# Performance work log

Measured on AMD Instinct MI355X. Metric: run time of the kernel, lower is better.

## Reference

```python
import jax, jax.numpy as jnp
import numpy as np

N_A, N_B = 50000, 10000
E = 300000
IN_F, HID, BEL_OUT, INC_OUT = 256, 256, 128, 128


def _gconv(x_src, W, b, src, dst, n_src, n_dst):
    """DGL GraphConv with norm='both': D_in^{-1/2} A D_out^{-1/2} X W + b, degs clamped to >=1."""
    ones = jnp.ones(src.shape[0], x_src.dtype)
    deg_out = jnp.maximum(jax.ops.segment_sum(ones, src, num_segments=n_src), 1.0)
    deg_in = jnp.maximum(jax.ops.segment_sum(ones, dst, num_segments=n_dst), 1.0)
    h = (x_src * jax.lax.rsqrt(deg_out)[:, None]) @ W        # [n_src, out]
    agg = jax.ops.segment_sum(h[src], dst, num_segments=n_dst)  # scatter-add messages
    return agg * jax.lax.rsqrt(deg_in)[:, None] + b


def setup_inputs() -> dict:
    key = jax.random.key(0)
    ks = jax.random.split(key, 12)
    s = 1.0 / np.sqrt(IN_F)
    sh = 1.0 / np.sqrt(HID)
    return {
        "x_a": jax.random.normal(ks[0], (N_A, IN_F), jnp.float32),
        "x_b": jax.random.normal(ks[1], (N_B, IN_F), jnp.float32),
        "W1_bel": jax.random.normal(ks[2], (IN_F, HID), jnp.float32) * s,
        "b1_bel": jnp.zeros((HID,), jnp.float32),
        "W1_inc": jax.random.normal(ks[3], (IN_F, HID), jnp.float32) * s,
        "b1_inc": jnp.zeros((HID,), jnp.float32),
        "W2_bel": jax.random.normal(ks[4], (HID, BEL_OUT), jnp.float32) * sh,
        "b2_bel": jnp.zeros((BEL_OUT,), jnp.float32),
        "W2_inc": jax.random.normal(ks[5], (HID, INC_OUT), jnp.float32) * sh,
        "b2_inc": jnp.zeros((INC_OUT,), jnp.float32),
        "bel_src": jax.random.randint(ks[6], (E,), 0, N_A, jnp.int32),
        "bel_dst": jax.random.randint(ks[7], (E,), 0, N_B, jnp.int32),
        "inc_src": jax.random.randint(ks[8], (E,), 0, N_B, jnp.int32),
        "inc_dst": jax.random.randint(ks[9], (E,), 0, N_A, jnp.int32),
    }


def reference(x_a, x_b, W1_bel, b1_bel, W1_inc, b1_inc, W2_bel, b2_bel,
              W2_inc, b2_inc, bel_src, bel_dst, inc_src, inc_dst):
    n_a, n_b = x_a.shape[0], x_b.shape[0]
    # layer 1 (HeteroGraphConv, mean over a single relation per dst type = identity)
    h_b = _gconv(x_a, W1_bel, b1_bel, bel_src, bel_dst, n_a, n_b)  # 'belongs_to': A->B
    h_a = _gconv(x_b, W1_inc, b1_inc, inc_src, inc_dst, n_b, n_a)  # 'including' : B->A
    h_a = jax.nn.relu(h_a)
    h_b = jax.nn.relu(h_b)
    # layer 2
    out_b = _gconv(h_a, W2_bel, b2_bel, bel_src, bel_dst, n_a, n_b)  # [N_B, bel_out]
    out_a = _gconv(h_b, W2_inc, b2_inc, inc_src, inc_dst, n_b, n_a)  # [N_A, inc_out]
    return out_a, out_b
```

## Files before the change

kernel.cpp:

```cpp
#include <hip/hip_runtime.h>


#define NA 50000
#define NB 10000
#define NE 300000
#define HB 1172
#define CVTB 400

typedef unsigned short u16;
typedef unsigned int u32;
typedef __attribute__((ext_vector_type(8))) short short8;
typedef __attribute__((ext_vector_type(4))) float f32x4;
typedef __attribute__((ext_vector_type(2))) float f32x2;
typedef __attribute__((ext_vector_type(4))) unsigned short u16x4;

__device__ __forceinline__ float bf2f(u16 h){
  union { u32 u; float f; } x; x.u = ((u32)h) << 16; return x.f;
}
__device__ __forceinline__ u16 f2bf(float f){
  union { float f; u32 u; } x; x.f = f;
  u32 r = (x.u + 0x7FFFu + ((x.u >> 16) & 1u)) >> 16;
  return (u16)r;
}

__global__ __launch_bounds__(256) void setup0_kernel(
    int* __restrict__ z, int nz,
    const float* __restrict__ W1b, const float* __restrict__ W1i,
    const float* __restrict__ W2b, const float* __restrict__ W2i,
    u16* __restrict__ pwh, u16* __restrict__ pwl){
  int g = blockIdx.x * blockDim.x + threadIdx.x;
  int s = gridDim.x * blockDim.x;
  for (int i = g; i < nz; i += s) z[i] = 0;
  const int total = 65536 + 65536 + 32768 + 32768;
  for (int t = g; t < total; t += s){
    const float* W; int N; int tt;
    if (t < 65536)       { W = W1b; N = 256; tt = t; }
    else if (t < 131072) { W = W1i; N = 256; tt = t - 65536; }
    else if (t < 163840) { W = W2b; N = 128; tt = t - 131072; }
    else                 { W = W2i; N = 128; tt = t - 163840; }
    int j = tt & 7, lane = (tt >> 3) & 63, tile = tt >> 9;
    int nT = N >> 4;
    int nt = tile % nT, kt = tile / nT;
    int k = kt * 32 + ((lane >> 4) << 3) + j;
    int n = nt * 16 + (lane & 15);
    float v = W[k * N + n];
    u16 hi = f2bf(v);
    pwh[t] = hi;
    pwl[t] = f2bf(v - bf2f(hi));
  }
}

__global__ __launch_bounds__(256) void histcvt_kernel(
    const int* __restrict__ bs, const int* __restrict__ bd,
    const int* __restrict__ isc, const int* __restrict__ idt,
    int* __restrict__ c_bs, int* __restrict__ c_bd,
    int* __restrict__ c_is, int* __restrict__ c_id,
    int* __restrict__ rank_bel, int* __restrict__ rank_inc,
    const float* __restrict__ xa, u16* __restrict__ xa16){
  if (blockIdx.x < HB){
    int g = blockIdx.x * blockDim.x + threadIdx.x;
    int s = HB * blockDim.x;
    for (int e = g; e < NE; e += s){
      atomicAdd(&c_bs[bs[e]], 1);
      rank_bel[e] = atomicAdd(&c_bd[bd[e]], 1);
      atomicAdd(&c_is[isc[e]], 1);
      rank_inc[e] = atomicAdd(&c_id[idt[e]], 1);
    }
  } else {
    int g = ((blockIdx.x - HB) * blockDim.x + threadIdx.x) * 4;
    int s = CVTB * blockDim.x * 4;
    for (int i = g; i < NA * 256; i += s){
      float4 v = *(const float4*)(xa + i);
      u16x4 o;
      o.x = f2bf(v.x); o.y = f2bf(v.y); o.z = f2bf(v.z); o.w = f2bf(v.w);
      __builtin_nontemporal_store(o, (u16x4*)(xa16 + i));
    }
  }
}

__global__ __launch_bounds__(1024) void scan_scales_kernel(
    const int* __restrict__ c_bs, const int* __restrict__ c_bd,
    const int* __restrict__ c_is, const int* __restrict__ c_id,
    int* __restrict__ off_bel, int* __restrict__ off_inc,
    float* __restrict__ s_ob, float* __restrict__ s_ib,
    float* __restrict__ s_oi, float* __restrict__ s_ii){
  if (blockIdx.x >= 2){
    int g = (blockIdx.x - 2) * blockDim.x + threadIdx.x;
    int s = (gridDim.x - 2) * blockDim.x;
    for (int i = g; i < NA; i += s){
      int a = c_bs[i]; s_ob[i] = rsqrtf((float)(a > 1 ? a : 1));
      int b = c_id[i]; s_ii[i] = rsqrtf((float)(b > 1 ? b : 1));
      if (i < NB){
        int c = c_bd[i]; s_ib[i] = rsqrtf((float)(c > 1 ? c : 1));
        int d = c_is[i]; s_oi[i] = rsqrtf((float)(d > 1 ? d : 1));
      }
    }
    return;
  }
  const int* cnt; int* off; int n;
  if (blockIdx.x == 0){ cnt = c_bd; off = off_bel; n = NB; }
  else                { cnt = c_id; off = off_inc; n = NA; }
  __shared__ int wsum[16];
  __shared__ int carry, chunkTot;
  int tid = threadIdx.x, lane = tid & 63, wid = tid >> 6;
  if (tid == 0) carry = 0;
  __syncthreads();
  for (int base = 0; base < n; base += 4096){
    int i0 = base + tid * 4;
    int v[4];
#pragma unroll
    for (int r = 0; r < 4; ++r){ int idx = i0 + r; v[r] = (idx < n) ? cnt[idx] : 0; }
    int s = v[0] + v[1] + v[2] + v[3];
    int x = s;
#pragma unroll
    for (int d = 1; d < 64; d <<= 1){ int t = __shfl_up(x, d, 64); if (lane >= d) x += t; }
    if (lane == 63) wsum[wid] = x;
    __syncthreads();
    if (wid == 0){
      int ws = (lane < 16) ? wsum[lane] : 0;
#pragma unroll
      for (int d = 1; d < 16; d <<= 1){ int t = __shfl_up(ws, d, 64); if (lane >= d) ws += t; }
      if (lane < 16) wsum[lane] = ws;
      if (lane == 15) chunkTot = ws;
    }
    __syncthreads();
    int waveBase = (wid == 0) ? 0 : wsum[wid - 1];
    int run = carry + waveBase + (x - s);
#pragma unroll
    for (int r = 0; r < 4; ++r){ int idx = i0 + r; if (idx < n) off[idx] = run; run += v[r]; }
    __syncthreads();
    if (tid == 0) carry += chunkTot;
    __syncthreads();
  }
  if (tid == 0) off[n] = carry;
}

__global__ __launch_bounds__(256) void fill_kernel(
    const int* __restrict__ bs, const int* __restrict__ bd,
    const int* __restrict__ isc, const int* __restrict__ idt,
    const int* __restrict__ rank_bel, const int* __restrict__ rank_inc,
    const int* __restrict__ off_bel, const int* __restrict__ off_inc,
    int* __restrict__ csr_bel, int* __restrict__ csr_inc){
  int g = blockIdx.x * blockDim.x + threadIdx.x;
  int s = gridDim.x * blockDim.x;
  for (int e = g; e < NE; e += s){
    csr_bel[off_bel[bd[e]] + rank_bel[e]] = bs[e];
    csr_inc[off_inc[idt[e]] + rank_inc[e]] = isc[e];
  }
}

__global__ __launch_bounds__(256) void agg_bel_kernel(
    const u16* __restrict__ X, const float* __restrict__ ss,
    const int* __restrict__ off, const int* __restrict__ csr,
    float* __restrict__ Pf, int nDst){
  int wave = blockIdx.x * 4 + (threadIdx.x >> 6);
  int lane = threadIdx.x & 63;
  if (wave >= nDst) return;
  int b0 = off[wave], b1 = off[wave + 1];
  int deg = b1 - b0;
  int part = lane >> 5;
  int cl = lane & 31;
  int c = cl * 8;
  float acc[8];
#pragma unroll
  for (int q = 0; q < 8; ++q) acc[q] = 0.f;
  int idx = 0; float sc = 0.f;
  if (lane < deg){
    idx = csr[b0 + lane];
    sc = ss ? ss[idx] : 1.f;
  }
  int lim = deg < 64 ? deg : 64;
  for (int u = 0; u < lim; u += 8){
    const u16* addr[4]; float w[4];
#pragma unroll
    for (int k = 0; k < 4; ++k){
      int e = u + k * 2 + part;
      int t = e < lim ? e : 0;
      int s0 = __shfl(idx, t, 64);
      float c0 = __shfl(sc, t, 64);
      w[k] = e < lim ? c0 : 0.f;
      addr[k] = X + (size_t)s0 * 256 + c;
    }
    short8 v[4];
#pragma unroll
    for (int k = 0; k < 4; ++k) v[k] = *(const short8*)addr[k];
#pragma unroll
    for (int k = 0; k < 4; ++k)
#pragma unroll
      for (int q = 0; q < 8; ++q) acc[q] += bf2f((u16)v[k][q]) * w[k];
  }
  for (int j = b0 + 64 + part; j < b1; j += 2){
    int s0 = csr[j];
    float c0 = ss ? ss[s0] : 1.f;
    short8 v0 = *(const short8*)(X + (size_t)s0 * 256 + c);
#pragma unroll
    for (int q = 0; q < 8; ++q) acc[q] += bf2f((u16)v0[q]) * c0;
  }
#pragma unroll
  for (int q = 0; q < 8; ++q) acc[q] += __shfl_xor(acc[q], 32, 64);
  if (part == 0){
    f32x4 f0 = {acc[0], acc[1], acc[2], acc[3]};
    f32x4 f1 = {acc[4], acc[5], acc[6], acc[7]};
    __builtin_nontemporal_store(f0, (f32x4*)(Pf + (size_t)wave * 256 + c));
    __builtin_nontemporal_store(f1, (f32x4*)(Pf + (size_t)wave * 256 + c + 4));
  }
}

__global__ __launch_bounds__(256) void agg_inc2_kernel(
    const u16* __restrict__ G12, const int* __restrict__ off,
    const int* __restrict__ csr,
    const float* __restrict__ s_ii, const float* __restrict__ s_ob,
    const float* __restrict__ b1i, const float* __restrict__ b2i,
    u16* __restrict__ Ha, float* __restrict__ outa){
  int wave = blockIdx.x * 4 + (threadIdx.x >> 6);
  int lane = threadIdx.x & 63;
  if (wave >= NA) return;
  int b0 = off[wave], b1 = off[wave + 1];
  int deg = b1 - b0;
  int c1 = lane * 4;
  int c2 = lane * 2;
  float acc[6];
#pragma unroll
  for (int q = 0; q < 6; ++q) acc[q] = 0.f;
  int idx = 0;
  if (lane < deg) idx = csr[b0 + lane];
  int lim = deg < 64 ? deg : 64;
  for (int u = 0; u < lim; u += 4){
    ushort4 va[4]; ushort2 vb[4]; float w[4];
#pragma unroll
    for (int k = 0; k < 4; ++k){
      int e = u + k;
      int t = e < lim ? e : 0;
      int se = __shfl(idx, t, 64);
      w[k] = e < lim ? 1.f : 0.f;
      const u16* r = G12 + (size_t)se * 384;
      va[k] = *(const ushort4*)(r + c1);
      vb[k] = *(const ushort2*)(r + 256 + c2);
    }
#pragma unroll
    for (int k = 0; k < 4; ++k){
      acc[0] += bf2f(va[k].x) * w[k];
      acc[1] += bf2f(va[k].y) * w[k];
      acc[2] += bf2f(va[k].z) * w[k];
      acc[3] += bf2f(va[k].w) * w[k];
      acc[4] += bf2f(vb[k].x) * w[k];
      acc[5] += bf2f(vb[k].y) * w[k];
    }
  }
  for (int j = b0 + 64; j < b1; ++j){
    int se = csr[j];
    const u16* r = G12 + (size_t)se * 384;
    ushort4 va = *(const ushort4*)(r + c1);
    ushort2 vb = *(const ushort2*)(r + 256 + c2);
    acc[0] += bf2f(va.x); acc[1] += bf2f(va.y);
    acc[2] += bf2f(va.z); acc[3] += bf2f(va.w);
    acc[4] += bf2f(vb.x); acc[5] += bf2f(vb.y);
  }
  float sii = s_ii[wave], sob = s_ob[wave];
  float4 bb1 = *(const float4*)(b1i + c1);
  f32x2 bb2 = *(const f32x2*)(b2i + c2);
  u16x4 o1;
  o1.x = f2bf(fmaxf(acc[0] * sii + bb1.x, 0.f) * sob);
  o1.y = f2bf(fmaxf(acc[1] * sii + bb1.y, 0.f) * sob);
  o1.z = f2bf(fmaxf(acc[2] * sii + bb1.z, 0.f) * sob);
  o1.w = f2bf(fmaxf(acc[3] * sii + bb1.w, 0.f) * sob);
  __builtin_nontemporal_store(o1, (u16x4*)(Ha + (size_t)wave * 256 + c1));
  f32x2 o2 = {acc[4] * sii + bb2.x, acc[5] * sii + bb2.y};
  __builtin_nontemporal_store(o2, (f32x2*)(outa + (size_t)wave * 128 + c2));
}

__global__ __launch_bounds__(256) void gemm_kernel(
    const float* __restrict__ A,
    const u16* __restrict__ PWH, const u16* __restrict__ PWL,
    const float* __restrict__ bias, const float* __restrict__ rs,
    float* __restrict__ Cf, u16* __restrict__ C16,
    int M, int nT, int wpsShift, int doRelu, int ldC, int colOff){
  int wave = blockIdx.x * 4 + (threadIdx.x >> 6);
  int lane = threadIdx.x & 63;
  int strips = M >> 4;
  int strip = wave >> wpsShift;
  if (strip >= strips) return;
  int slice = wave & ((1 << wpsShift) - 1);
  int ntPer = nT >> wpsShift;
  int ntStart = slice * ntPer;
  int r16 = lane & 15, quad = lane >> 4;
  int m0 = strip << 4;
  const float* aBase = A + (size_t)(m0 + r16) * 256 + quad * 8;
  short8 ah[8], al[8];
#pragma unroll
  for (int kt = 0; kt < 8; ++kt){
    float4 p0 = *(const float4*)(aBase + kt * 32);
    float4 p1 = *(const float4*)(aBase + kt * 32 + 4);
    float v[8] = {p0.x, p0.y, p0.z, p0.w, p1.x, p1.y, p1.z, p1.w};
    short8 h, l;
#pragma unroll
    for (int j = 0; j < 8; ++j){
      u16 hb = f2bf(v[j]);
      h[j] = (short)hb;
      l[j] = (short)f2bf(v[j] - bf2f(hb));
    }
    ah[kt] = h; al[kt] = l;
  }
  float rscale[4];
#pragma unroll
  for (int r = 0; r < 4; ++r) rscale[r] = rs ? rs[m0 + quad * 4 + r] : 1.f;
  for (int nt = ntStart; nt < ntStart + ntPer; ++nt){
    f32x4 acc = {0.f, 0.f, 0.f, 0.f};
    const u16* bh = PWH + ((size_t)nt * 64 + lane) * 8;
    const u16* bl = PWL + ((size_t)nt * 64 + lane) * 8;
#pragma unroll
    for (int kt = 0; kt < 8; ++kt){
      short8 wh = *(const short8*)(bh + (size_t)kt * nT * 512);
      short8 wl = *(const short8*)(bl + (size_t)kt * nT * 512);
      acc = __builtin_amdgcn_mfma_f32_16x16x32_bf16(ah[kt], wh, acc, 0, 0, 0);
      acc = __builtin_amdgcn_mfma_f32_16x16x32_bf16(al[kt], wh, acc, 0, 0, 0);
      acc = __builtin_amdgcn_mfma_f32_16x16x32_bf16(ah[kt], wl, acc, 0, 0, 0);
    }
    int col = nt * 16 + r16;
    float bv = bias ? bias[col] : 0.f;
#pragma unroll
    for (int r = 0; r < 4; ++r){
      float v = acc[r] * rscale[r] + bv;
      if (doRelu) v = fmaxf(v, 0.f);
      size_t o = (size_t)(m0 + quad * 4 + r) * ldC + colOff + col;
      if (C16) __builtin_nontemporal_store(f2bf(v), C16 + o);
      else     __builtin_nontemporal_store(v, Cf + o);
    }
  }
}

extern "C" void kernel_launch(void* const* d_in, const int* in_sizes, int n_in,
                              void* d_out, int out_size, void* d_ws, size_t ws_size,
                              hipStream_t stream){
  const float* x_a = (const float*)d_in[0];
  const float* x_b = (const float*)d_in[1];
  const float* W1b = (const float*)d_in[2];
  const float* b1b = (const float*)d_in[3];
  const float* W1i = (const float*)d_in[4];
  const float* b1i = (const float*)d_in[5];
  const float* W2b = (const float*)d_in[6];
  const float* b2b = (const float*)d_in[7];
  const float* W2i = (const float*)d_in[8];
  const float* b2i = (const float*)d_in[9];
  const int* bs  = (const int*)d_in[10];
  const int* bd  = (const int*)d_in[11];
  const int* isc = (const int*)d_in[12];
  const int* idt = (const int*)d_in[13];

  char* w = (char*)d_ws;
  size_t o = 0;
  auto take = [&](size_t bytes) -> void* {
    void* p = w + o; o = (o + bytes + 255) & ~(size_t)255; return p;
  };
  int* zint = (int*)take(120000 * sizeof(int));
  int* c_bs = zint, *c_bd = zint + 50000, *c_is = zint + 60000, *c_id = zint + 70000;
  int* rank_bel = (int*)take(NE * sizeof(int));
  int* rank_inc = (int*)take(NE * sizeof(int));
  int* off_bel = (int*)take((NB + 1) * sizeof(int));
  int* off_inc = (int*)take((NA + 1) * sizeof(int));
  int* csr_bel = (int*)take(NE * sizeof(int));
  int* csr_inc = (int*)take(NE * sizeof(int));
  float* s_ob = (float*)take(NA * sizeof(float));
  float* s_ib = (float*)take(NB * sizeof(float));
  float* s_oi = (float*)take(NB * sizeof(float));
  float* s_ii = (float*)take(NA * sizeof(float));
  u16* pwh = (u16*)take(196608 * sizeof(u16));
  u16* pwl = (u16*)take(196608 * sizeof(u16));
  u16* pwh1b = pwh, *pwh1i = pwh + 65536, *pwh2b = pwh + 131072, *pwh2i = pwh + 163840;
  u16* pwl1b = pwl, *pwl1i = pwl + 65536, *pwl2b = pwl + 131072, *pwl2i = pwl + 163840;
  u16* xa16 = (u16*)take((size_t)NA * 256 * sizeof(u16));
  u16* G12  = (u16*)take((size_t)NB * 384 * sizeof(u16));
  u16* H_a  = (u16*)take((size_t)NA * 256 * sizeof(u16));
  float* P_b = (float*)take((size_t)NB * 256 * sizeof(float));
  float* H_b = (float*)take((size_t)NB * 256 * sizeof(float));

  float* out_a = (float*)d_out;
  float* out_b = (float*)d_out + (size_t)NA * 128;

  setup0_kernel<<<512, 256, 0, stream>>>(zint, 120000, W1b, W1i, W2b, W2i, pwh, pwl);
  histcvt_kernel<<<HB + CVTB, 256, 0, stream>>>(bs, bd, isc, idt,
                                                c_bs, c_bd, c_is, c_id,
                                                rank_bel, rank_inc, x_a, xa16);
  scan_scales_kernel<<<52, 1024, 0, stream>>>(c_bs, c_bd, c_is, c_id,
                                              off_bel, off_inc,
                                              s_ob, s_ib, s_oi, s_ii);
  fill_kernel<<<1172, 256, 0, stream>>>(bs, bd, isc, idt, rank_bel, rank_inc,
                                        off_bel, off_inc, csr_bel, csr_inc);

  gemm_kernel<<<625, 256, 0, stream>>>(x_b, pwh1i, pwl1i, nullptr, s_oi,
                                       nullptr, G12, NB, 16, 2, 0, 384, 0);
  agg_bel_kernel<<<2500, 256, 0, stream>>>(xa16, s_ob, off_bel, csr_bel, P_b, NB);
  gemm_kernel<<<625, 256, 0, stream>>>(P_b, pwh1b, pwl1b, b1b, s_ib,
                                       H_b, nullptr, NB, 16, 2, 1, 256, 0);
  gemm_kernel<<<625, 256, 0, stream>>>(H_b, pwh2i, pwl2i, nullptr, s_oi,
                                       nullptr, G12, NB, 8, 2, 0, 384, 256);
  agg_inc2_kernel<<<12500, 256, 0, stream>>>(G12, off_inc, csr_inc,
                                             s_ii, s_ob, b1i, b2i, H_a, out_a);
  agg_bel_kernel<<<2500, 256, 0, stream>>>(H_a, nullptr, off_bel, csr_bel, P_b, NB);
  gemm_kernel<<<625, 256, 0, stream>>>(P_b, pwh2b, pwl2b, b2b, s_ib,
                                       out_b, nullptr, NB, 8, 2, 0, 128, 0);
}
```

Before: 409.4 us.

## Fuse back-to-back GEMMs via shared memory and merge small launches

The two chained GEMMs (P_b·W1b with ReLU, then H_b·W2i) become one kernel that keeps the 16-row H_b tile in LDS, so the fp32 H_b round trip through global memory is gone. The x_b GEMM is co-scheduled with the CSR fill in one launch, and the x_a bf16 conversion moves into the setup kernel while the histogram gets its own kernel. This cuts two kernel launches and an intermediate buffer, in exchange for LDS use and a different block split between the merged workloads.

New measurement: 354.9 us. -13.3%, faster.

```diff
diff --git a/kernel.cpp b/kernel.cpp
--- a/kernel.cpp
+++ b/kernel.cpp
@@ -4,8 +4,6 @@
 #define NA 50000
 #define NB 10000
 #define NE 300000
-#define HB 1172
-#define CVTB 400
 
 typedef unsigned short u16;
 typedef unsigned int u32;
@@ -27,7 +25,8 @@
     int* __restrict__ z, int nz,
     const float* __restrict__ W1b, const float* __restrict__ W1i,
     const float* __restrict__ W2b, const float* __restrict__ W2i,
-    u16* __restrict__ pwh, u16* __restrict__ pwl){
+    u16* __restrict__ pwh, u16* __restrict__ pwl,
+    const float* __restrict__ xa, u16* __restrict__ xa16){
   int g = blockIdx.x * blockDim.x + threadIdx.x;
   int s = gridDim.x * blockDim.x;
   for (int i = g; i < nz; i += s) z[i] = 0;
@@ -48,33 +47,27 @@
     pwh[t] = hi;
     pwl[t] = f2bf(v - bf2f(hi));
   }
-}
-
-__global__ __launch_bounds__(256) void histcvt_kernel(
+  for (int i = g * 4; i < NA * 256; i += s * 4){
+    float4 v = *(const float4*)(xa + i);
+    u16x4 o;
+    o.x = f2bf(v.x); o.y = f2bf(v.y); o.z = f2bf(v.z); o.w = f2bf(v.w);
+    __builtin_nontemporal_store(o, (u16x4*)(xa16 + i));
+  }
+}
+
+__global__ __launch_bounds__(256) void hist_kernel(
     const int* __restrict__ bs, const int* __restrict__ bd,
     const int* __restrict__ isc, const int* __restrict__ idt,
     int* __restrict__ c_bs, int* __restrict__ c_bd,
     int* __restrict__ c_is, int* __restrict__ c_id,
-    int* __restrict__ rank_bel, int* __restrict__ rank_inc,
-    const float* __restrict__ xa, u16* __restrict__ xa16){
-  if (blockIdx.x < HB){
-    int g = blockIdx.x * blockDim.x + threadIdx.x;
-    int s = HB * blockDim.x;
-    for (int e = g; e < NE; e += s){
-      atomicAdd(&c_bs[bs[e]], 1);
-      rank_bel[e] = atomicAdd(&c_bd[bd[e]], 1);
-      atomicAdd(&c_is[isc[e]], 1);
-      rank_inc[e] = atomicAdd(&c_id[idt[e]], 1);
-    }
-  } else {
-    int g = ((blockIdx.x - HB) * blockDim.x + threadIdx.x) * 4;
-    int s = CVTB * blockDim.x * 4;
-    for (int i = g; i < NA * 256; i += s){
-      float4 v = *(const float4*)(xa + i);
-      u16x4 o;
-      o.x = f2bf(v.x); o.y = f2bf(v.y); o.z = f2bf(v.z); o.w = f2bf(v.w);
-      __builtin_nontemporal_store(o, (u16x4*)(xa16 + i));
-    }
+    int* __restrict__ rank_bel, int* __restrict__ rank_inc){
+  int g = blockIdx.x * blockDim.x + threadIdx.x;
+  int s = gridDim.x * blockDim.x;
+  for (int e = g; e < NE; e += s){
+    atomicAdd(&c_bs[bs[e]], 1);
+    rank_bel[e] = atomicAdd(&c_bd[bd[e]], 1);
+    atomicAdd(&c_is[isc[e]], 1);
+    rank_inc[e] = atomicAdd(&c_id[idt[e]], 1);
   }
 }
 
@@ -135,17 +128,176 @@
   if (tid == 0) off[n] = carry;
 }
 
-__global__ __launch_bounds__(256) void fill_kernel(
+__device__ __forceinline__ void gemm_dev(int blk, const float* __restrict__ A,
+                                         const u16* __restrict__ PWH,
+                                         const u16* __restrict__ PWL,
+                                         const float* __restrict__ bias,
+                                         const float* __restrict__ rs,
+                                         float* __restrict__ Cf,
+                                         u16* __restrict__ C16,
+                                         int M, int nT, int wpsShift,
+                                         int doRelu, int ldC, int colOff){
+  int wave = blk * 4 + (threadIdx.x >> 6);
+  int lane = threadIdx.x & 63;
+  int strips = M >> 4;
+  int strip = wave >> wpsShift;
+  if (strip >= strips) return;
+  int slice = wave & ((1 << wpsShift) - 1);
+  int ntPer = nT >> wpsShift;
+  int ntStart = slice * ntPer;
+  int r16 = lane & 15, quad = lane >> 4;
+  int m0 = strip << 4;
+  const float* aBase = A + (size_t)(m0 + r16) * 256 + quad * 8;
+  short8 ah[8], al[8];
+#pragma unroll
+  for (int kt = 0; kt < 8; ++kt){
+    float4 p0 = *(const float4*)(aBase + kt * 32);
+    float4 p1 = *(const float4*)(aBase + kt * 32 + 4);
+    float v[8] = {p0.x, p0.y, p0.z, p0.w, p1.x, p1.y, p1.z, p1.w};
+    short8 h, l;
+#pragma unroll
+    for (int j = 0; j < 8; ++j){
+      u16 hb = f2bf(v[j]);
+      h[j] = (short)hb;
+      l[j] = (short)f2bf(v[j] - bf2f(hb));
+    }
+    ah[kt] = h; al[kt] = l;
+  }
+  float rscale[4];
+#pragma unroll
+  for (int r = 0; r < 4; ++r) rscale[r] = rs ? rs[m0 + quad * 4 + r] : 1.f;
+  for (int nt = ntStart; nt < ntStart + ntPer; ++nt){
+    f32x4 acc = {0.f, 0.f, 0.f, 0.f};
+    const u16* bh = PWH + ((size_t)nt * 64 + lane) * 8;
+    const u16* bl = PWL + ((size_t)nt * 64 + lane) * 8;
+#pragma unroll
+    for (int kt = 0; kt < 8; ++kt){
+      short8 wh = *(const short8*)(bh + (size_t)kt * nT * 512);
+      short8 wl = *(const short8*)(bl + (size_t)kt * nT * 512);
+      acc = __builtin_amdgcn_mfma_f32_16x16x32_bf16(ah[kt], wh, acc, 0, 0, 0);
+      acc = __builtin_amdgcn_mfma_f32_16x16x32_bf16(al[kt], wh, acc, 0, 0, 0);
+      acc = __builtin_amdgcn_mfma_f32_16x16x32_bf16(ah[kt], wl, acc, 0, 0, 0);
+    }
+    int col = nt * 16 + r16;
+    float bv = bias ? bias[col] : 0.f;
+#pragma unroll
+    for (int r = 0; r < 4; ++r){
+      float v = acc[r] * rscale[r] + bv;
+      if (doRelu) v = fmaxf(v, 0.f);
+      size_t o = (size_t)(m0 + quad * 4 + r) * ldC + colOff + col;
+      if (C16) __builtin_nontemporal_store(f2bf(v), C16 + o);
+      else     __builtin_nontemporal_store(v, Cf + o);
+    }
+  }
+}
+
+__global__ __launch_bounds__(256) void fillg1_kernel(
+    const float* __restrict__ xb,
+    const u16* __restrict__ WH1i, const u16* __restrict__ WL1i,
+    const float* __restrict__ s_oi, u16* __restrict__ G12,
     const int* __restrict__ bs, const int* __restrict__ bd,
     const int* __restrict__ isc, const int* __restrict__ idt,
     const int* __restrict__ rank_bel, const int* __restrict__ rank_inc,
     const int* __restrict__ off_bel, const int* __restrict__ off_inc,
     int* __restrict__ csr_bel, int* __restrict__ csr_inc){
-  int g = blockIdx.x * blockDim.x + threadIdx.x;
-  int s = gridDim.x * blockDim.x;
-  for (int e = g; e < NE; e += s){
-    csr_bel[off_bel[bd[e]] + rank_bel[e]] = bs[e];
-    csr_inc[off_inc[idt[e]] + rank_inc[e]] = isc[e];
+  if (blockIdx.x < 625){
+    gemm_dev(blockIdx.x, xb, WH1i, WL1i, nullptr, s_oi,
+             nullptr, G12, NB, 16, 2, 0, 384, 0);
+  } else {
+    int g = (blockIdx.x - 625) * blockDim.x + threadIdx.x;
+    int s = (gridDim.x - 625) * blockDim.x;
+    for (int e = g; e < NE; e += s){
+      csr_bel[off_bel[bd[e]] + rank_bel[e]] = bs[e];
+      csr_inc[off_inc[idt[e]] + rank_inc[e]] = isc[e];
+    }
+  }
+}
+
+__global__ __launch_bounds__(256) void gemmHG_kernel(
+    const float* __restrict__ Pb,
+    const u16* __restrict__ WH1b, const u16* __restrict__ WL1b,
+    const float* __restrict__ b1b, const float* __restrict__ s_ib,
+    const u16* __restrict__ WH2i, const u16* __restrict__ WL2i,
+    const float* __restrict__ s_oi, u16* __restrict__ G12){
+  __shared__ float Hs[16][260];
+  int w = threadIdx.x >> 6;
+  int lane = threadIdx.x & 63;
+  int r16 = lane & 15, quad = lane >> 4;
+  int m0 = blockIdx.x << 4;
+  const float* aBase = Pb + (size_t)(m0 + r16) * 256 + quad * 8;
+  short8 ah[8], al[8];
+#pragma unroll
+  for (int kt = 0; kt < 8; ++kt){
+    float4 p0 = *(const float4*)(aBase + kt * 32);
+    float4 p1 = *(const float4*)(aBase + kt * 32 + 4);
+    float v[8] = {p0.x, p0.y, p0.z, p0.w, p1.x, p1.y, p1.z, p1.w};
+    short8 h, l;
+#pragma unroll
+    for (int j = 0; j < 8; ++j){
+      u16 hb = f2bf(v[j]);
+      h[j] = (short)hb;
+      l[j] = (short)f2bf(v[j] - bf2f(hb));
+    }
+    ah[kt] = h; al[kt] = l;
+  }
+  float rs1[4];
+#pragma unroll
+  for (int r = 0; r < 4; ++r) rs1[r] = s_ib[m0 + quad * 4 + r];
+  for (int nt = w * 4; nt < w * 4 + 4; ++nt){
+    f32x4 acc = {0.f, 0.f, 0.f, 0.f};
+    const u16* bh = WH1b + ((size_t)nt * 64 + lane) * 8;
+    const u16* bl = WL1b + ((size_t)nt * 64 + lane) * 8;
+#pragma unroll
+    for (int kt = 0; kt < 8; ++kt){
+      short8 wh = *(const short8*)(bh + (size_t)kt * 16 * 512);
+      short8 wl = *(const short8*)(bl + (size_t)kt * 16 * 512);
+      acc = __builtin_amdgcn_mfma_f32_16x16x32_bf16(ah[kt], wh, acc, 0, 0, 0);
+      acc = __builtin_amdgcn_mfma_f32_16x16x32_bf16(al[kt], wh, acc, 0, 0, 0);
+      acc = __builtin_amdgcn_mfma_f32_16x16x32_bf16(ah[kt], wl, acc, 0, 0, 0);
+    }
+    int col = nt * 16 + r16;
+    float bv = b1b[col];
+#pragma unroll
+    for (int r = 0; r < 4; ++r)
+      Hs[quad * 4 + r][col] = fmaxf(acc[r] * rs1[r] + bv, 0.f);
+  }
+  __syncthreads();
+  short8 ah2[8], al2[8];
+#pragma unroll
+  for (int kt = 0; kt < 8; ++kt){
+    float4 p0 = *(const float4*)&Hs[r16][kt * 32 + quad * 8];
+    float4 p1 = *(const float4*)&Hs[r16][kt * 32 + quad * 8 + 4];
+    float v[8] = {p0.x, p0.y, p0.z, p0.w, p1.x, p1.y, p1.z, p1.w};
+    short8 h, l;
+#pragma unroll
+    for (int j = 0; j < 8; ++j){
+      u16 hb = f2bf(v[j]);
+      h[j] = (short)hb;
+      l[j] = (short)f2bf(v[j] - bf2f(hb));
+    }
+    ah2[kt] = h; al2[kt] = l;
+  }
+  float rs2[4];
+#pragma unroll
+  for (int r = 0; r < 4; ++r) rs2[r] = s_oi[m0 + quad * 4 + r];
+  for (int nt = w * 2; nt < w * 2 + 2; ++nt){
+    f32x4 acc = {0.f, 0.f, 0.f, 0.f};
+    const u16* bh = WH2i + ((size_t)nt * 64 + lane) * 8;
+    const u16* bl = WL2i + ((size_t)nt * 64 + lane) * 8;
+#pragma unroll
+    for (int kt = 0; kt < 8; ++kt){
+      short8 wh = *(const short8*)(bh + (size_t)kt * 8 * 512);
+      short8 wl = *(const short8*)(bl + (size_t)kt * 8 * 512);
+      acc = __builtin_amdgcn_mfma_f32_16x16x32_bf16(ah2[kt], wh, acc, 0, 0, 0);
+      acc = __builtin_amdgcn_mfma_f32_16x16x32_bf16(al2[kt], wh, acc, 0, 0, 0);
+      acc = __builtin_amdgcn_mfma_f32_16x16x32_bf16(ah2[kt], wl, acc, 0, 0, 0);
+    }
+    int col = nt * 16 + r16;
+#pragma unroll
+    for (int r = 0; r < 4; ++r){
+      u16 o = f2bf(acc[r] * rs2[r]);
+      __builtin_nontemporal_store(o, G12 + (size_t)(m0 + quad * 4 + r) * 384 + 256 + col);
+    }
   }
 }
 
@@ -275,58 +427,8 @@
     const float* __restrict__ bias, const float* __restrict__ rs,
     float* __restrict__ Cf, u16* __restrict__ C16,
     int M, int nT, int wpsShift, int doRelu, int ldC, int colOff){
-  int wave = blockIdx.x * 4 + (threadIdx.x >> 6);
-  int lane = threadIdx.x & 63;
-  int strips = M >> 4;
-  int strip = wave >> wpsShift;
-  if (strip >= strips) return;
-  int slice = wave & ((1 << wpsShift) - 1);
-  int ntPer = nT >> wpsShift;
-  int ntStart = slice * ntPer;
-  int r16 = lane & 15, quad = lane >> 4;
-  int m0 = strip << 4;
-  const float* aBase = A + (size_t)(m0 + r16) * 256 + quad * 8;
-  short8 ah[8], al[8];
-#pragma unroll
-  for (int kt = 0; kt < 8; ++kt){
-    float4 p0 = *(const float4*)(aBase + kt * 32);
-    float4 p1 = *(const float4*)(aBase + kt * 32 + 4);
-    float v[8] = {p0.x, p0.y, p0.z, p0.w, p1.x, p1.y, p1.z, p1.w};
-    short8 h, l;
-#pragma unroll
-    for (int j = 0; j < 8; ++j){
-      u16 hb = f2bf(v[j]);
-      h[j] = (short)hb;
-      l[j] = (short)f2bf(v[j] - bf2f(hb));
-    }
-    ah[kt] = h; al[kt] = l;
-  }
-  float rscale[4];
-#pragma unroll
-  for (int r = 0; r < 4; ++r) rscale[r] = rs ? rs[m0 + quad * 4 + r] : 1.f;
-  for (int nt = ntStart; nt < ntStart + ntPer; ++nt){
-    f32x4 acc = {0.f, 0.f, 0.f, 0.f};
-    const u16* bh = PWH + ((size_t)nt * 64 + lane) * 8;
-    const u16* bl = PWL + ((size_t)nt * 64 + lane) * 8;
-#pragma unroll
-    for (int kt = 0; kt < 8; ++kt){
-      short8 wh = *(const short8*)(bh + (size_t)kt * nT * 512);
-      short8 wl = *(const short8*)(bl + (size_t)kt * nT * 512);
-      acc = __builtin_amdgcn_mfma_f32_16x16x32_bf16(ah[kt], wh, acc, 0, 0, 0);
-      acc = __builtin_amdgcn_mfma_f32_16x16x32_bf16(al[kt], wh, acc, 0, 0, 0);
-      acc = __builtin_amdgcn_mfma_f32_16x16x32_bf16(ah[kt], wl, acc, 0, 0, 0);
-    }
-    int col = nt * 16 + r16;
-    float bv = bias ? bias[col] : 0.f;
-#pragma unroll
-    for (int r = 0; r < 4; ++r){
-      float v = acc[r] * rscale[r] + bv;
-      if (doRelu) v = fmaxf(v, 0.f);
-      size_t o = (size_t)(m0 + quad * 4 + r) * ldC + colOff + col;
-      if (C16) __builtin_nontemporal_store(f2bf(v), C16 + o);
-      else     __builtin_nontemporal_store(v, Cf + o);
-    }
-  }
+  gemm_dev(blockIdx.x, A, PWH, PWL, bias, rs, Cf, C16,
+           M, nT, wpsShift, doRelu, ldC, colOff);
 }
 
 extern "C" void kernel_launch(void* const* d_in, const int* in_sizes, int n_in,
@@ -372,28 +474,26 @@
   u16* G12  = (u16*)take((size_t)NB * 384 * sizeof(u16));
   u16* H_a  = (u16*)take((size_t)NA * 256 * sizeof(u16));
   float* P_b = (float*)take((size_t)NB * 256 * sizeof(float));
-  float* H_b = (float*)take((size_t)NB * 256 * sizeof(float));
 
   float* out_a = (float*)d_out;
   float* out_b = (float*)d_out + (size_t)NA * 128;
 
-  setup0_kernel<<<512, 256, 0, stream>>>(zint, 120000, W1b, W1i, W2b, W2i, pwh, pwl);
-  histcvt_kernel<<<HB + CVTB, 256, 0, stream>>>(bs, bd, isc, idt,
-                                                c_bs, c_bd, c_is, c_id,
-                                                rank_bel, rank_inc, x_a, xa16);
+  setup0_kernel<<<1024, 256, 0, stream>>>(zint, 120000, W1b, W1i, W2b, W2i,
+                                          pwh, pwl, x_a, xa16);
+  hist_kernel<<<1172, 256, 0, stream>>>(bs, bd, isc, idt,
+                                        c_bs, c_bd, c_is, c_id,
+                                        rank_bel, rank_inc);
   scan_scales_kernel<<<52, 1024, 0, stream>>>(c_bs, c_bd, c_is, c_id,
                                               off_bel, off_inc,
                                               s_ob, s_ib, s_oi, s_ii);
-  fill_kernel<<<1172, 256, 0, stream>>>(bs, bd, isc, idt, rank_bel, rank_inc,
-                                        off_bel, off_inc, csr_bel, csr_inc);
-
-  gemm_kernel<<<625, 256, 0, stream>>>(x_b, pwh1i, pwl1i, nullptr, s_oi,
-                                       nullptr, G12, NB, 16, 2, 0, 384, 0);
+  fillg1_kernel<<<625 + 1172, 256, 0, stream>>>(x_b, pwh1i, pwl1i, s_oi, G12,
+                                                bs, bd, isc, idt,
+                                                rank_bel, rank_inc,
+                                                off_bel, off_inc,
+                                                csr_bel, csr_inc);
   agg_bel_kernel<<<2500, 256, 0, stream>>>(xa16, s_ob, off_bel, csr_bel, P_b, NB);
-  gemm_kernel<<<625, 256, 0, stream>>>(P_b, pwh1b, pwl1b, b1b, s_ib,
-                                       H_b, nullptr, NB, 16, 2, 1, 256, 0);
-  gemm_kernel<<<625, 256, 0, stream>>>(H_b, pwh2i, pwl2i, nullptr, s_oi,
-                                       nullptr, G12, NB, 8, 2, 0, 384, 256);
+  gemmHG_kernel<<<625, 256, 0, stream>>>(P_b, pwh1b, pwl1b, b1b, s_ib,
+                                         pwh2i, pwl2i, s_oi, G12);
   agg_inc2_kernel<<<12500, 256, 0, stream>>>(G12, off_inc, csr_inc,
                                              s_ii, s_ob, b1i, b2i, H_a, out_a);
   agg_bel_kernel<<<2500, 256, 0, stream>>>(H_a, nullptr, off_bel, csr_bel, P_b, NB);
```
